# Kernel optimization log

Hardware: AMD Instinct MI355X
Metric: run time of the kernel (lower is better)

The kernel has to match this reference:

```python
import jax, jax.numpy as jnp
import numpy as np

IN_DIM = 256
OUT_DIM = 256
NUM_HEADS = 4
HEAD_DIM = OUT_DIM // NUM_HEADS
N_SRC = 100000
N_DST = 50000
N_EDGES = 300000


def setup_inputs() -> dict:
    key = jax.random.key(0)
    ks = jax.random.split(key, 10)
    h_src = jax.random.normal(ks[0], (N_SRC, IN_DIM), dtype=jnp.float32)
    h_dst = jax.random.normal(ks[1], (N_DST, IN_DIM), dtype=jnp.float32)
    src_idx = jax.random.randint(ks[2], (N_EDGES,), 0, N_SRC)
    dst_idx = jax.random.randint(ks[3], (N_EDGES,), 0, N_DST)
    # torch nn.Linear weights are [out, in]; xavier-uniform init, zero bias
    def xavier(k, shape):
        limit = jnp.sqrt(6.0 / (shape[0] + shape[1]))
        return jax.random.uniform(k, shape, jnp.float32, -limit, limit)
    Wq = xavier(ks[4], (OUT_DIM, IN_DIM))
    Wk = xavier(ks[5], (OUT_DIM, IN_DIM))
    Wv = xavier(ks[6], (OUT_DIM, IN_DIM))
    bq = jnp.zeros((OUT_DIM,), jnp.float32)
    bk = jnp.zeros((OUT_DIM,), jnp.float32)
    bv = jnp.zeros((OUT_DIM,), jnp.float32)
    return {"h_src": h_src, "h_dst": h_dst, "src_idx": src_idx, "dst_idx": dst_idx,
            "Wq": Wq, "bq": bq, "Wk": Wk, "bk": bk, "Wv": Wv, "bv": bv}


def reference(h_src, h_dst, src_idx, dst_idx, Wq, bq, Wk, bk, Wv, bv):
    # Projections (torch Linear: x @ W.T + b), reshape to [N, H, Dh]
    Q = (h_dst @ Wq.T + bq).reshape(-1, NUM_HEADS, HEAD_DIM)
    K = (h_src @ Wk.T + bk).reshape(-1, NUM_HEADS, HEAD_DIM)
    V = (h_src @ Wv.T + bv).reshape(-1, NUM_HEADS, HEAD_DIM)

    # Edge scores: u_dot_v('K','Q') -> per-edge, per-head dot product [E, H]
    score = jnp.einsum('ehd,ehd->eh', K[src_idx], Q[dst_idx]) / jnp.sqrt(
        jnp.asarray(HEAD_DIM, jnp.float32))

    # Edge softmax grouped by destination (per head), numerically stable
    seg_max = jax.ops.segment_max(score, dst_idx, num_segments=N_DST)
    seg_max = jnp.where(jnp.isfinite(seg_max), seg_max, 0.0)
    e = jnp.exp(score - seg_max[dst_idx])
    seg_sum = jax.ops.segment_sum(e, dst_idx, num_segments=N_DST)
    a = e / seg_sum[dst_idx]  # [E, H]

    # Weighted sum aggregation: u_mul_e then sum per destination
    m = V[src_idx] * a[:, :, None]  # [E, H, Dh]
    h = jax.ops.segment_sum(m, dst_idx, num_segments=N_DST)  # [N_dst, H, Dh]
    return h.reshape(-1, OUT_DIM)
```

## Files before the change

### kernel.cpp

```cpp
#include <hip/hip_runtime.h>
#include <hip/hip_bf16.h>
#include <stdint.h>

#define IN_DIM    256
#define OUT_DIM   256
#define NUM_HEADS 4
#define HEAD_DIM  64
#define N_SRC     100000
#define N_DST     50000
#define N_EDGES   300000

#define BM 128
#define BN 256
#define BK 32
#define SCAN_NBLK ((N_DST + 1023) / 1024)

typedef __attribute__((ext_vector_type(8))) short v8s;
typedef __attribute__((ext_vector_type(4))) float v4f;

__device__ __forceinline__ unsigned short f2bf(float f) {
    unsigned u = __float_as_uint(f);
    unsigned r = (u + 0x7FFFu + ((u >> 16) & 1u)) >> 16;
    return (unsigned short)r;
}
__device__ __forceinline__ float bf2f(unsigned short s) {
    return __uint_as_float(((unsigned)s) << 16);
}

__device__ __forceinline__ void async_copy16(const unsigned short* g,
                                             unsigned short* l) {
    __builtin_amdgcn_global_load_lds(
        (const __attribute__((address_space(1))) unsigned int*)g,
        (__attribute__((address_space(3))) unsigned int*)l, 16, 0, 0);
}

__global__ void wcvt_kernel(const float* __restrict__ wq,
                            const float* __restrict__ wk,
                            const float* __restrict__ wv,
                            unsigned short* __restrict__ dst) {
    int i = blockIdx.x * 256 + threadIdx.x;
    if (i >= 3 * 8192) return;
    int m = i >> 13;
    int r = i & 8191;
    const float* s = (m == 0) ? wq : (m == 1) ? wk : wv;
    const float4* sp = (const float4*)(s + (size_t)r * 8);
    float4 x = sp[0], y = sp[1];
    v8s o;
    o[0] = (short)f2bf(x.x); o[1] = (short)f2bf(x.y);
    o[2] = (short)f2bf(x.z); o[3] = (short)f2bf(x.w);
    o[4] = (short)f2bf(y.x); o[5] = (short)f2bf(y.y);
    o[6] = (short)f2bf(y.z); o[7] = (short)f2bf(y.w);
    *(v8s*)(dst + (size_t)m * 65536 + (size_t)r * 8) = o;
}

__global__ __launch_bounds__(512, 2) void gemm_kernel(
    const float* __restrict__ h_src, const float* __restrict__ h_dst,
    const unsigned short* __restrict__ Wb,
    const float* __restrict__ bq, const float* __restrict__ bk,
    const float* __restrict__ bv,
    unsigned short* __restrict__ Q, unsigned short* __restrict__ K,
    unsigned short* __restrict__ V) {

    __shared__ unsigned short smem[24576];

    int z = blockIdx.z;
    const float* A; const unsigned short* W;
    const float* bias; unsigned short* Out; int M;
    if (z == 0)      { A = h_dst; W = Wb;          bias = bq; Out = Q; M = N_DST; }
    else if (z == 1) { A = h_src; W = Wb + 65536;  bias = bk; Out = K; M = N_SRC; }
    else             { A = h_src; W = Wb + 131072; bias = bv; Out = V; M = N_SRC; }

    int mbase = blockIdx.x * BM;
    if (mbase >= M) return;

    int tid  = threadIdx.x;
    int wave = tid >> 6, lane = tid & 63;
    int lm = lane & 15, quad = lane >> 4;
    int wrow = wave >> 2;
    int wcol = wave & 3;

    int ar = tid >> 2, akc = (tid & 3) * 8;
    int gr = mbase + ar; if (gr > M - 1) gr = M - 1;
    const float* gA = A + (size_t)gr * 256 + akc;

    int sr = lane >> 2, skc = (lane & 3) * 8;
    const unsigned short* gB0 = W + (size_t)(wave * 32 + sr) * 256 + skc;
    const unsigned short* gB1 = gB0 + (size_t)16 * 256;

    v4f acc[4][4];
#pragma unroll
    for (int i = 0; i < 4; i++)
#pragma unroll
        for (int j = 0; j < 4; j++) acc[i][j] = (v4f){0, 0, 0, 0};

    const int NK = 256 / BK;

    float4 xc, yc;
    {
        float4 x0 = *(const float4*)(gA);
        float4 y0 = *(const float4*)(gA + 4);
        async_copy16(gB0, &smem[8192 + (wave * 32) * 32]);
        async_copy16(gB1, &smem[8192 + (wave * 32 + 16) * 32]);
        xc = *(const float4*)(gA + BK);
        yc = *(const float4*)(gA + BK + 4);
        v8s o;
        o[0] = (short)f2bf(x0.x); o[1] = (short)f2bf(x0.y);
        o[2] = (short)f2bf(x0.z); o[3] = (short)f2bf(x0.w);
        o[4] = (short)f2bf(y0.x); o[5] = (short)f2bf(y0.y);
        o[6] = (short)f2bf(y0.z); o[7] = (short)f2bf(y0.w);
        *(v8s*)&smem[(size_t)ar * 32 + akc] = o;
        asm volatile("s_waitcnt vmcnt(2) lgkmcnt(0)" ::: "memory");
        __builtin_amdgcn_s_barrier();
        __builtin_amdgcn_sched_barrier(0);
    }

    int buf = 0;
#pragma unroll
    for (int ks = 0; ks < NK; ks++) {
        float4 xn, yn;
        if (ks + 1 < NK) {
            int k0 = (ks + 1) * BK;
            async_copy16(gB0 + k0,
                         &smem[8192 + (buf ^ 1) * 8192 + (wave * 32) * 32]);
            async_copy16(gB1 + k0,
                         &smem[8192 + (buf ^ 1) * 8192 + (wave * 32 + 16) * 32]);
        }
        if (ks + 2 < NK) {
            int k0 = (ks + 2) * BK;
            xn = *(const float4*)(gA + k0);
            yn = *(const float4*)(gA + k0 + 4);
        }

        const unsigned short* sAb = smem + buf * 4096;
        const unsigned short* sBb = smem + 8192 + buf * 8192;
        v8s af[4], bfr[4];
#pragma unroll
        for (int i = 0; i < 4; i++)
            af[i] = *(const v8s*)&sAb[(wrow * 64 + i * 16 + lm) * 32 + quad * 8];
#pragma unroll
        for (int j = 0; j < 4; j++)
            bfr[j] = *(const v8s*)&sBb[(wcol * 64 + j * 16 + lm) * 32 + quad * 8];
#pragma unroll
        for (int i = 0; i < 4; i++)
#pragma unroll
            for (int j = 0; j < 4; j++)
                acc[i][j] = __builtin_amdgcn_mfma_f32_16x16x32_bf16(
                    af[i], bfr[j], acc[i][j], 0, 0, 0);

        if (ks + 1 < NK) {
            v8s o;
            o[0] = (short)f2bf(xc.x); o[1] = (short)f2bf(xc.y);
            o[2] = (short)f2bf(xc.z); o[3] = (short)f2bf(xc.w);
            o[4] = (short)f2bf(yc.x); o[5] = (short)f2bf(yc.y);
            o[6] = (short)f2bf(yc.z); o[7] = (short)f2bf(yc.w);
            *(v8s*)&smem[(buf ^ 1) * 4096 + (size_t)ar * 32 + akc] = o;
            if (ks + 2 < NK)
                asm volatile("s_waitcnt vmcnt(2) lgkmcnt(0)" ::: "memory");
            else
                asm volatile("s_waitcnt vmcnt(0) lgkmcnt(0)" ::: "memory");
            __builtin_amdgcn_s_barrier();
            __builtin_amdgcn_sched_barrier(0);
        }
        xc = xn; yc = yn;
        buf ^= 1;
    }

#pragma unroll
    for (int p = 0; p < 2; p++) {
        __syncthreads();
        if (wrow == p) {
#pragma unroll
            for (int j = 0; j < 4; j++) {
                int col = wcol * 64 + j * 16 + lm;
                float bcol = bias[col];
#pragma unroll
                for (int i = 0; i < 4; i++)
#pragma unroll
                    for (int r = 0; r < 4; r++)
                        smem[(i * 16 + quad * 4 + r) * 256 + col] =
                            f2bf(acc[i][j][r] + bcol);
            }
        }
        __syncthreads();
#pragma unroll
        for (int k = 0; k < 4; k++) {
            int c = tid + k * 512;
            int rl = c >> 5, ch = c & 31;
            int grow = mbase + p * 64 + rl;
            if (grow < M)
                *(v8s*)(Out + (size_t)grow * 256 + ch * 8) =
                    *(const v8s*)&smem[rl * 256 + ch * 8];
        }
    }
}

__global__ void hist_kernel(const int* __restrict__ dst_idx,
                            int* __restrict__ cnt) {
    int i = blockIdx.x * 256 + threadIdx.x;
    if (i < N_EDGES) atomicAdd(&cnt[dst_idx[i]], 1);
}

__global__ __launch_bounds__(1024) void scan_local_kernel(
    const int* __restrict__ cnt, int* __restrict__ offsets,
    int* __restrict__ bsum) {
    __shared__ int wsum[16];
    int t = threadIdx.x, b = blockIdx.x;
    int i = b * 1024 + t;
    int lane = t & 63, w = t >> 6;
    int v = (i < N_DST) ? cnt[i] : 0;
    int s = v;
#pragma unroll
    for (int off = 1; off < 64; off <<= 1) {
        int u = __shfl_up(s, off, 64);
        if (lane >= off) s += u;
    }
    if (lane == 63) wsum[w] = s;
    __syncthreads();
    if (w == 0) {
        int x = (lane < 16) ? wsum[lane] : 0;
#pragma unroll
        for (int off = 1; off < 16; off <<= 1) {
            int u = __shfl_up(x, off, 64);
            if (lane >= off) x += u;
        }
        if (lane < 16) wsum[lane] = x;
    }
    __syncthreads();
    int wbase = (w == 0) ? 0 : wsum[w - 1];
    if (i < N_DST) offsets[i] = wbase + s - v;
    if (t == 1023) bsum[b] = wsum[15];
}

__global__ void scan_base_kernel(int* __restrict__ bsum,
                                 int* __restrict__ offsets) {
    int lane = threadIdx.x;
    int v = (lane < SCAN_NBLK) ? bsum[lane] : 0;
    int s = v;
#pragma unroll
    for (int off = 1; off < 64; off <<= 1) {
        int u = __shfl_up(s, off, 64);
        if (lane >= off) s += u;
    }
    if (lane < SCAN_NBLK) bsum[lane] = s - v;
    if (lane == 0) offsets[N_DST] = N_EDGES;
}

__global__ __launch_bounds__(1024) void scan_fixup_kernel(
    int* __restrict__ offsets, int* __restrict__ cursor,
    const int* __restrict__ bsum) {
    int i = blockIdx.x * 1024 + threadIdx.x;
    if (i >= N_DST) return;
    int off = offsets[i] + bsum[i >> 10];
    offsets[i] = off;
    cursor[i] = off;
}

__global__ void scatter_kernel(const int* __restrict__ src_idx,
                               const int* __restrict__ dst_idx,
                               int* __restrict__ cursor,
                               int* __restrict__ esrc) {
    int i = blockIdx.x * 256 + threadIdx.x;
    if (i >= N_EDGES) return;
    int d = dst_idx[i];
    int pos = atomicAdd(&cursor[d], 1);
    esrc[pos] = src_idx[i];
}

__global__ __launch_bounds__(256) void agg_kernel(
    const int* __restrict__ esrc, const int* __restrict__ offsets,
    const unsigned short* __restrict__ Q, const unsigned short* __restrict__ K,
    const unsigned short* __restrict__ V, float* __restrict__ out) {

    int wave = threadIdx.x >> 6, lane = threadIdx.x & 63;
    int d = blockIdx.x * 4 + wave;
    if (d >= N_DST) return;

    int start = offsets[d], end = offsets[d + 1];
    float4 o = make_float4(0.f, 0.f, 0.f, 0.f);

    if (end > start) {
        ushort4 qv = *((const ushort4*)(Q + (size_t)d * 256) + lane);
        float q0 = bf2f(qv.x), q1 = bf2f(qv.y), q2 = bf2f(qv.z), q3 = bf2f(qv.w);

        float m = -3.0e38f, l = 0.f;
        float a0 = 0.f, a1 = 0.f, a2 = 0.f, a3 = 0.f;

        int s0 = esrc[start];
        int sN = (start + 1 < end) ? esrc[start + 1] : 0;
        ushort4 kv = *((const ushort4*)(K + (size_t)s0 * 256) + lane);
        ushort4 vv = *((const ushort4*)(V + (size_t)s0 * 256) + lane);

        for (int j = start; j < end; j++) {
            ushort4 kc = kv, vc = vv;
            int sNN = (j + 2 < end) ? esrc[j + 2] : 0;
            if (j + 1 < end) {
                kv = *((const ushort4*)(K + (size_t)sN * 256) + lane);
                vv = *((const ushort4*)(V + (size_t)sN * 256) + lane);
            }
            sN = sNN;

            float p = bf2f(kc.x) * q0 + bf2f(kc.y) * q1 +
                      bf2f(kc.z) * q2 + bf2f(kc.w) * q3;
            p += __shfl_xor(p, 1, 64);
            p += __shfl_xor(p, 2, 64);
            p += __shfl_xor(p, 4, 64);
            p += __shfl_xor(p, 8, 64);
            p *= 0.125f;

            float mn = fmaxf(m, p);
            float sc = __expf(m - mn);
            float w  = __expf(p - mn);
            l = l * sc + w;
            a0 = a0 * sc + w * bf2f(vc.x);
            a1 = a1 * sc + w * bf2f(vc.y);
            a2 = a2 * sc + w * bf2f(vc.z);
            a3 = a3 * sc + w * bf2f(vc.w);
            m = mn;
        }
        float inv = 1.0f / l;
        o = make_float4(a0 * inv, a1 * inv, a2 * inv, a3 * inv);
    }
    *((float4*)(out + (size_t)d * 256) + lane) = o;
}

extern "C" void kernel_launch(void* const* d_in, const int* in_sizes, int n_in,
                              void* d_out, int out_size, void* d_ws, size_t ws_size,
                              hipStream_t stream) {
    const float* h_src   = (const float*)d_in[0];
    const float* h_dst   = (const float*)d_in[1];
    const int*   src_idx = (const int*)d_in[2];
    const int*   dst_idx = (const int*)d_in[3];
    const float* Wq      = (const float*)d_in[4];
    const float* bq      = (const float*)d_in[5];
    const float* Wk      = (const float*)d_in[6];
    const float* bk      = (const float*)d_in[7];
    const float* Wv      = (const float*)d_in[8];
    const float* bv      = (const float*)d_in[9];
    float* out = (float*)d_out;

    char* ws = (char*)d_ws;
    size_t off = 0;
    auto take = [&](size_t bytes) { char* p = ws + off; off = (off + bytes + 255) & ~(size_t)255; return p; };
    unsigned short* Q       = (unsigned short*)take((size_t)N_DST * 256 * 2);
    unsigned short* K       = (unsigned short*)take((size_t)N_SRC * 256 * 2);
    unsigned short* V       = (unsigned short*)take((size_t)N_SRC * 256 * 2);
    unsigned short* Wb      = (unsigned short*)take((size_t)3 * 65536 * 2);
    int*            cnt     = (int*)take((size_t)N_DST * 4);
    int*            offsets = (int*)take((size_t)(N_DST + 1) * 4);
    int*            cursor  = (int*)take((size_t)N_DST * 4);
    int*            esrc    = (int*)take((size_t)N_EDGES * 4);
    int*            bsum    = (int*)take((size_t)64 * 4);
    (void)ws_size; (void)in_sizes; (void)n_in; (void)out_size;

    hipMemsetAsync(cnt, 0, (size_t)N_DST * 4, stream);

    wcvt_kernel<<<96, 256, 0, stream>>>(Wq, Wk, Wv, Wb);

    hist_kernel<<<(N_EDGES + 255) / 256, 256, 0, stream>>>(dst_idx, cnt);
    scan_local_kernel<<<SCAN_NBLK, 1024, 0, stream>>>(cnt, offsets, bsum);
    scan_base_kernel<<<1, 64, 0, stream>>>(bsum, offsets);
    scan_fixup_kernel<<<SCAN_NBLK, 1024, 0, stream>>>(offsets, cursor, bsum);
    scatter_kernel<<<(N_EDGES + 255) / 256, 256, 0, stream>>>(src_idx, dst_idx, cursor, esrc);

    gemm_kernel<<<dim3((N_SRC + BM - 1) / BM, 1, 3), 512, 0, stream>>>(
        h_src, h_dst, Wb, bq, bk, bv, Q, K, V);

    agg_kernel<<<(N_DST + 3) / 4, 256, 0, stream>>>(esrc, offsets, Q, K, V, out);
}
```

Measured before the change: 347.0 us.

## Deepen GEMM prefetch pipeline to triple-buffered B and three-stage A loads

Changes the projection GEMM from double-buffered to triple-buffered weight tiles in LDS, and prefetches A rows three k-steps ahead instead of two, with hand-tuned vmcnt waits per iteration. The aim is to hide more global-memory latency behind the MFMA work. In exchange, LDS use grows from 48KB to 64KB per block, which may limit occupancy at 2 blocks per CU. More prefetch registers are also live, and the hand-counted waits are fragile.

New measurement: 360.8 us. 1.04x slower.

```diff
diff --git a/kernel.cpp b/kernel.cpp
--- a/kernel.cpp
+++ b/kernel.cpp
@@ -61,7 +61,7 @@
     unsigned short* __restrict__ Q, unsigned short* __restrict__ K,
     unsigned short* __restrict__ V) {
 
-    __shared__ unsigned short smem[24576];
+    __shared__ unsigned short smem[32768];
 
     int z = blockIdx.z;
     const float* A; const unsigned short* W;
@@ -95,44 +95,50 @@
 
     const int NK = 256 / BK;
 
-    float4 xc, yc;
+    float4 xc, yc, xn, yn;
     {
         float4 x0 = *(const float4*)(gA);
         float4 y0 = *(const float4*)(gA + 4);
-        async_copy16(gB0, &smem[8192 + (wave * 32) * 32]);
-        async_copy16(gB1, &smem[8192 + (wave * 32 + 16) * 32]);
+        async_copy16(gB0,      &smem[8192 + (wave * 32) * 32]);
+        async_copy16(gB1,      &smem[8192 + (wave * 32 + 16) * 32]);
+        async_copy16(gB0 + BK, &smem[8192 + 8192 + (wave * 32) * 32]);
+        async_copy16(gB1 + BK, &smem[8192 + 8192 + (wave * 32 + 16) * 32]);
+        __builtin_amdgcn_sched_barrier(0);
         xc = *(const float4*)(gA + BK);
         yc = *(const float4*)(gA + BK + 4);
+        xn = *(const float4*)(gA + 2 * BK);
+        yn = *(const float4*)(gA + 2 * BK + 4);
         v8s o;
         o[0] = (short)f2bf(x0.x); o[1] = (short)f2bf(x0.y);
         o[2] = (short)f2bf(x0.z); o[3] = (short)f2bf(x0.w);
         o[4] = (short)f2bf(y0.x); o[5] = (short)f2bf(y0.y);
         o[6] = (short)f2bf(y0.z); o[7] = (short)f2bf(y0.w);
         *(v8s*)&smem[(size_t)ar * 32 + akc] = o;
-        asm volatile("s_waitcnt vmcnt(2) lgkmcnt(0)" ::: "memory");
+        asm volatile("s_waitcnt vmcnt(6) lgkmcnt(0)" ::: "memory");
         __builtin_amdgcn_s_barrier();
         __builtin_amdgcn_sched_barrier(0);
     }
 
-    int buf = 0;
 #pragma unroll
     for (int ks = 0; ks < NK; ks++) {
-        float4 xn, yn;
-        if (ks + 1 < NK) {
-            int k0 = (ks + 1) * BK;
-            async_copy16(gB0 + k0,
-                         &smem[8192 + (buf ^ 1) * 8192 + (wave * 32) * 32]);
-            async_copy16(gB1 + k0,
-                         &smem[8192 + (buf ^ 1) * 8192 + (wave * 32 + 16) * 32]);
-        }
+        float4 xm, ym;
         if (ks + 2 < NK) {
             int k0 = (ks + 2) * BK;
-            xn = *(const float4*)(gA + k0);
-            yn = *(const float4*)(gA + k0 + 4);
-        }
-
-        const unsigned short* sAb = smem + buf * 4096;
-        const unsigned short* sBb = smem + 8192 + buf * 8192;
+            int bslot = (ks + 2) % 3;
+            async_copy16(gB0 + k0,
+                         &smem[8192 + bslot * 8192 + (wave * 32) * 32]);
+            async_copy16(gB1 + k0,
+                         &smem[8192 + bslot * 8192 + (wave * 32 + 16) * 32]);
+        }
+        __builtin_amdgcn_sched_barrier(0);
+        if (ks + 3 < NK) {
+            int k0 = (ks + 3) * BK;
+            xm = *(const float4*)(gA + k0);
+            ym = *(const float4*)(gA + k0 + 4);
+        }
+
+        const unsigned short* sAb = smem + (ks & 1) * 4096;
+        const unsigned short* sBb = smem + 8192 + (ks % 3) * 8192;
         v8s af[4], bfr[4];
 #pragma unroll
         for (int i = 0; i < 4; i++)
@@ -153,16 +159,19 @@
             o[2] = (short)f2bf(xc.z); o[3] = (short)f2bf(xc.w);
             o[4] = (short)f2bf(yc.x); o[5] = (short)f2bf(yc.y);
             o[6] = (short)f2bf(yc.z); o[7] = (short)f2bf(yc.w);
-            *(v8s*)&smem[(buf ^ 1) * 4096 + (size_t)ar * 32 + akc] = o;
-            if (ks + 2 < NK)
-                asm volatile("s_waitcnt vmcnt(2) lgkmcnt(0)" ::: "memory");
-            else
-                asm volatile("s_waitcnt vmcnt(0) lgkmcnt(0)" ::: "memory");
+            *(v8s*)&smem[((ks + 1) & 1) * 4096 + (size_t)ar * 32 + akc] = o;
+        }
+        if (ks <= 4)
+            asm volatile("s_waitcnt vmcnt(6) lgkmcnt(0)" ::: "memory");
+        else if (ks == 5)
+            asm volatile("s_waitcnt vmcnt(4) lgkmcnt(0)" ::: "memory");
+        else if (ks == 6)
+            asm volatile("s_waitcnt vmcnt(0) lgkmcnt(0)" ::: "memory");
+        if (ks < NK - 1) {
             __builtin_amdgcn_s_barrier();
             __builtin_amdgcn_sched_barrier(0);
         }
-        xc = xn; yc = yn;
-        buf ^= 1;
+        xc = xn; yc = yn; xn = xm; yn = ym;
     }
 
 #pragma unroll
```

## Fold memset and scan fixup into neighboring kernels, deepen agg prefetch

Applied to the files above, without the earlier changes.

The cnt memset is folded into extra blocks of the weight-conversion kernel. The separate scan fixup kernel is removed: block-local offsets seed the cursors directly, and scatter and agg add the per-block base from bsum when they read them. The aggregation loop now prefetches one more edge index ahead so the K/V loads for the next edge are already issued. Together these remove two launches and one pass over offsets, at the cost of an extra bsum lookup per edge in scatter and per destination in agg.

Measured after the change: 344.1 us. Within noise of the previous version (-0.9%).

```diff
diff --git a/kernel.cpp b/kernel.cpp
--- a/kernel.cpp
+++ b/kernel.cpp
@@ -14,6 +14,7 @@
 #define BN 256
 #define BK 32
 #define SCAN_NBLK ((N_DST + 1023) / 1024)
+#define WCVT_BLKS 96
 
 typedef __attribute__((ext_vector_type(8))) short v8s;
 typedef __attribute__((ext_vector_type(4))) float v4f;
@@ -37,7 +38,13 @@
 __global__ void wcvt_kernel(const float* __restrict__ wq,
                             const float* __restrict__ wk,
                             const float* __restrict__ wv,
-                            unsigned short* __restrict__ dst) {
+                            unsigned short* __restrict__ dst,
+                            int* __restrict__ cnt) {
+    if (blockIdx.x >= WCVT_BLKS) {
+        int i = (blockIdx.x - WCVT_BLKS) * 1024 + threadIdx.x * 4;
+        if (i < N_DST) *(int4*)(cnt + i) = make_int4(0, 0, 0, 0);
+        return;
+    }
     int i = blockIdx.x * 256 + threadIdx.x;
     if (i >= 3 * 8192) return;
     int m = i >> 13;
@@ -202,7 +209,7 @@
 
 __global__ __launch_bounds__(1024) void scan_local_kernel(
     const int* __restrict__ cnt, int* __restrict__ offsets,
-    int* __restrict__ bsum) {
+    int* __restrict__ cursor, int* __restrict__ bsum) {
     __shared__ int wsum[16];
     int t = threadIdx.x, b = blockIdx.x;
     int i = b * 1024 + t;
@@ -227,12 +234,15 @@
     }
     __syncthreads();
     int wbase = (w == 0) ? 0 : wsum[w - 1];
-    if (i < N_DST) offsets[i] = wbase + s - v;
+    if (i < N_DST) {
+        int e = wbase + s - v;
+        offsets[i] = e;
+        cursor[i] = e;
+    }
     if (t == 1023) bsum[b] = wsum[15];
 }
 
-__global__ void scan_base_kernel(int* __restrict__ bsum,
-                                 int* __restrict__ offsets) {
+__global__ void scan_base_kernel(int* __restrict__ bsum) {
     int lane = threadIdx.x;
     int v = (lane < SCAN_NBLK) ? bsum[lane] : 0;
     int s = v;
@@ -242,32 +252,23 @@
         if (lane >= off) s += u;
     }
     if (lane < SCAN_NBLK) bsum[lane] = s - v;
-    if (lane == 0) offsets[N_DST] = N_EDGES;
-}
-
-__global__ __launch_bounds__(1024) void scan_fixup_kernel(
-    int* __restrict__ offsets, int* __restrict__ cursor,
-    const int* __restrict__ bsum) {
-    int i = blockIdx.x * 1024 + threadIdx.x;
-    if (i >= N_DST) return;
-    int off = offsets[i] + bsum[i >> 10];
-    offsets[i] = off;
-    cursor[i] = off;
 }
 
 __global__ void scatter_kernel(const int* __restrict__ src_idx,
                                const int* __restrict__ dst_idx,
                                int* __restrict__ cursor,
+                               const int* __restrict__ bsum,
                                int* __restrict__ esrc) {
     int i = blockIdx.x * 256 + threadIdx.x;
     if (i >= N_EDGES) return;
     int d = dst_idx[i];
-    int pos = atomicAdd(&cursor[d], 1);
+    int pos = atomicAdd(&cursor[d], 1) + bsum[d >> 10];
     esrc[pos] = src_idx[i];
 }
 
 __global__ __launch_bounds__(256) void agg_kernel(
     const int* __restrict__ esrc, const int* __restrict__ offsets,
+    const int* __restrict__ bsum,
     const unsigned short* __restrict__ Q, const unsigned short* __restrict__ K,
     const unsigned short* __restrict__ V, float* __restrict__ out) {
 
@@ -275,7 +276,9 @@
     int d = blockIdx.x * 4 + wave;
     if (d >= N_DST) return;
 
-    int start = offsets[d], end = offsets[d + 1];
+    int start = offsets[d] + bsum[d >> 10];
+    int end = (d + 1 == N_DST) ? N_EDGES
+                               : offsets[d + 1] + bsum[(d + 1) >> 10];
     float4 o = make_float4(0.f, 0.f, 0.f, 0.f);
 
     if (end > start) {
@@ -285,19 +288,23 @@
         float m = -3.0e38f, l = 0.f;
         float a0 = 0.f, a1 = 0.f, a2 = 0.f, a3 = 0.f;
 
-        int s0 = esrc[start];
-        int sN = (start + 1 < end) ? esrc[start + 1] : 0;
-        ushort4 kv = *((const ushort4*)(K + (size_t)s0 * 256) + lane);
-        ushort4 vv = *((const ushort4*)(V + (size_t)s0 * 256) + lane);
+        int n = end - start;
+        int i0 = esrc[start];
+        int i1 = (n > 1) ? esrc[start + 1] : i0;
+        int i2 = (n > 2) ? esrc[start + 2] : i0;
+        ushort4 k0 = *((const ushort4*)(K + (size_t)i0 * 256) + lane);
+        ushort4 v0 = *((const ushort4*)(V + (size_t)i0 * 256) + lane);
+        ushort4 k1 = *((const ushort4*)(K + (size_t)i1 * 256) + lane);
+        ushort4 v1 = *((const ushort4*)(V + (size_t)i1 * 256) + lane);
 
         for (int j = start; j < end; j++) {
-            ushort4 kc = kv, vc = vv;
-            int sNN = (j + 2 < end) ? esrc[j + 2] : 0;
-            if (j + 1 < end) {
-                kv = *((const ushort4*)(K + (size_t)sN * 256) + lane);
-                vv = *((const ushort4*)(V + (size_t)sN * 256) + lane);
+            ushort4 kc = k0, vc = v0;
+            k0 = k1; v0 = v1;
+            if (j + 2 < end) {
+                k1 = *((const ushort4*)(K + (size_t)i2 * 256) + lane);
+                v1 = *((const ushort4*)(V + (size_t)i2 * 256) + lane);
             }
-            sN = sNN;
+            i2 = (j + 3 < end) ? esrc[j + 3] : 0;
 
             float p = bf2f(kc.x) * q0 + bf2f(kc.y) * q1 +
                       bf2f(kc.z) * q2 + bf2f(kc.w) * q3;
@@ -352,18 +359,16 @@
     int*            bsum    = (int*)take((size_t)64 * 4);
     (void)ws_size; (void)in_sizes; (void)n_in; (void)out_size;
 
-    hipMemsetAsync(cnt, 0, (size_t)N_DST * 4, stream);
-
-    wcvt_kernel<<<96, 256, 0, stream>>>(Wq, Wk, Wv, Wb);
+    wcvt_kernel<<<WCVT_BLKS + SCAN_NBLK, 256, 0, stream>>>(Wq, Wk, Wv, Wb, cnt);
 
     hist_kernel<<<(N_EDGES + 255) / 256, 256, 0, stream>>>(dst_idx, cnt);
-    scan_local_kernel<<<SCAN_NBLK, 1024, 0, stream>>>(cnt, offsets, bsum);
-    scan_base_kernel<<<1, 64, 0, stream>>>(bsum, offsets);
-    scan_fixup_kernel<<<SCAN_NBLK, 1024, 0, stream>>>(offsets, cursor, bsum);
-    scatter_kernel<<<(N_EDGES + 255) / 256, 256, 0, stream>>>(src_idx, dst_idx, cursor, esrc);
+    scan_local_kernel<<<SCAN_NBLK, 1024, 0, stream>>>(cnt, offsets, cursor, bsum);
+    scan_base_kernel<<<1, 64, 0, stream>>>(bsum);
+    scatter_kernel<<<(N_EDGES + 255) / 256, 256, 0, stream>>>(src_idx, dst_idx,
+                                                              cursor, bsum, esrc);
 
     gemm_kernel<<<dim3((N_SRC + BM - 1) / BM, 1, 3), 512, 0, stream>>>(
         h_src, h_dst, Wb, bq, bk, bv, Q, K, V);
 
-    agg_kernel<<<(N_DST + 3) / 4, 256, 0, stream>>>(esrc, offsets, Q, K, V, out);
-}
+    agg_kernel<<<(N_DST + 3) / 4, 256, 0, stream>>>(esrc, offsets, bsum, Q, K, V, out);
+}
```
